# Kernel tuning notes

Hardware: AMD Instinct MI355X
Metric: run time of the kernel (lower is better)

Reference implementation:

```python
import jax, jax.numpy as jnp
import numpy as np

N_NODES = 100000
N_EDGES = 1600000
N_GRAPHS = 256
D = 128
L = 3
N_OUT = 10


def setup_inputs() -> dict:
    key = jax.random.key(0)
    ks = jax.random.split(key, 6)
    x = jax.random.normal(ks[0], (N_NODES, D), dtype=jnp.float32)
    edge_index = jax.random.randint(ks[1], (2, N_EDGES), 0, N_NODES, dtype=jnp.int64)
    batch = jnp.sort(jax.random.randint(ks[2], (N_NODES,), 0, N_GRAPHS, dtype=jnp.int64))
    conv_w = jax.random.normal(ks[3], (L, D, D), dtype=jnp.float32) * (1.0 / np.sqrt(D))
    conv_b = jnp.zeros((L, D), dtype=jnp.float32)
    out_w = jax.random.normal(ks[4], (3 * D, N_OUT), dtype=jnp.float32) * (1.0 / np.sqrt(3 * D))
    out_b = jnp.zeros((N_OUT,), dtype=jnp.float32)
    return {"x": x, "edge_index": edge_index, "batch": batch,
            "conv_w": conv_w, "conv_b": conv_b, "out_w": out_w, "out_b": out_b}


def reference(x, edge_index, batch, conv_w, conv_b, out_w, out_b):
    N = x.shape[0]
    # --- add self-loops (PyG GCNConv default) ---
    loop = jnp.arange(N, dtype=edge_index.dtype)
    src = jnp.concatenate([edge_index[0], loop])  # [E+N]
    dst = jnp.concatenate([edge_index[1], loop])
    # --- symmetric normalization: deg computed on dst (col) ---
    deg = jax.ops.segment_sum(jnp.ones_like(dst, dtype=x.dtype), dst, num_segments=N)
    dinv = jnp.where(deg > 0, jax.lax.rsqrt(jnp.maximum(deg, 1.0)), 0.0)
    norm = dinv[src] * dinv[dst]  # [E+N]

    h = x
    for l in range(conv_w.shape[0]):
        h = h @ conv_w[l]                                   # [N, D] transform first
        msg = h[src] * norm[:, None]                        # gather + scale
        h = jax.ops.segment_sum(msg, dst, num_segments=N)   # scatter-add
        h = jax.nn.relu(h + conv_b[l])

    # --- global max / mean / add pooling over graphs ---
    B = N_GRAPHS
    gmax = jax.ops.segment_max(h, batch, num_segments=B)
    gsum = jax.ops.segment_sum(h, batch, num_segments=B)
    cnt = jax.ops.segment_sum(jnp.ones((N, 1), h.dtype), batch, num_segments=B)
    gmean = gsum / jnp.maximum(cnt, 1.0)
    pooled = jnp.concatenate([gmax, gmean, gsum], axis=1)   # [B, 3D]
    # dropout p=0.5 is identity in eval mode
    return pooled @ out_w + out_b
```

## Files before the change

kernel.cpp:

```cpp
#include <hip/hip_runtime.h>
#include <hip/hip_bf16.h>

#define D 128
#define NP 8
#define DPB 64
#define KPB (DPB * NP)
#define SUB 64
#define CAP_SUB 64

typedef __attribute__((ext_vector_type(8))) __bf16 bf16x8;
typedef __attribute__((ext_vector_type(4))) float f32x4;
typedef __attribute__((ext_vector_type(4))) short s16x4;
typedef __attribute__((ext_vector_type(8))) short s16x8;

static __device__ __forceinline__ short f2bf(float f) {
    union { float f; unsigned u; } in; in.f = f;
    unsigned u = in.u;
    u += 0x7fffu + ((u >> 16) & 1u);
    return (short)(u >> 16);
}

__global__ void k_bucket(const int* __restrict__ src, const int* __restrict__ dst,
                         int* __restrict__ bcnt, int* __restrict__ staging,
                         int E, int KBE,
                         const float* __restrict__ W, short* __restrict__ Wt, int totw,
                         const int* __restrict__ batch, int* __restrict__ gstart,
                         int* __restrict__ gcnt, int N, int B) {
    const int EB = (E + 255) >> 8;
    if (blockIdx.x < (unsigned)EB) {
        int i = blockIdx.x * 256 + threadIdx.x;
        if (i >= E) return;
        int d = __builtin_nontemporal_load(dst + i);
        int s = __builtin_nontemporal_load(src + i);
        int b = d >> 6;
        int key = ((d & 63) << 3) | (s >> 14);
        int j = blockIdx.x & (SUB - 1);
        int slot = atomicAdd(&bcnt[j * KBE + b], 1);
        if (slot < CAP_SUB) staging[((size_t)j * KBE + b) * CAP_SUB + slot] = (key << 17) | s;
    } else if ((int)blockIdx.x - EB < (totw >> 8)) {
        int i = (blockIdx.x - EB) * 256 + threadIdx.x;
        if (i < totw) {
            int l = i >> 14;
            int rem = i & 16383;
            int n = rem >> 7;
            int k = rem & 127;
            Wt[i] = f2bf(W[(l << 14) + (k << 7) + n]);
        }
    } else {
        for (int g = threadIdx.x; g <= B; g += 256) {
            int lo = 0, hi = N;
            while (lo < hi) {
                int mid = (lo + hi) >> 1;
                if (batch[mid] < g) lo = mid + 1; else hi = mid;
            }
            gstart[g] = lo;
            if (g < B) {
                int lo2 = lo, hi2 = N;
                while (lo2 < hi2) {
                    int mid = (lo2 + hi2) >> 1;
                    if (batch[mid] < g + 1) lo2 = mid + 1; else hi2 = mid;
                }
                gcnt[g] = lo2 - lo;
            }
        }
    }
}

__global__ void k_bscan(const int* __restrict__ bcnt, int* __restrict__ bbase,
                        int* __restrict__ row_ptr, int nkeys, int KBE) {
    __shared__ int wtot[8];
    __shared__ int carry_s;
    const int t = threadIdx.x;
    const int w = t >> 6;
    const int lane = t & 63;
    if (t == 0) carry_s = 0;
    __syncthreads();
    for (int c0 = 0; c0 < KBE; c0 += 512) {
        const int b = c0 + t;
        int v = 0;
        if (b < KBE) {
            #pragma unroll 8
            for (int j = 0; j < SUB; j++) {
                int c = bcnt[j * KBE + b];
                v += (c > CAP_SUB) ? CAP_SUB : c;
            }
        }
        int is = v;
        #pragma unroll
        for (int off = 1; off < 64; off <<= 1) {
            int x = __shfl_up(is, off, 64);
            if (lane >= off) is += x;
        }
        if (lane == 63) wtot[w] = is;
        __syncthreads();
        if (t == 0) {
            int run = 0;
            #pragma unroll
            for (int i = 0; i < 8; i++) { int x = wtot[i]; wtot[i] = run; run += x; }
        }
        __syncthreads();
        const int excl = is - v + wtot[w] + carry_s;
        if (b < KBE) bbase[b] = excl;
        __syncthreads();
        if (t == 511) carry_s = excl + v;
        __syncthreads();
    }
    if (t == 0) { bbase[KBE] = carry_s; row_ptr[nkeys] = carry_s; }
}

__global__ __launch_bounds__(256) void k_build(
    const int* __restrict__ staging, const int* __restrict__ bcnt,
    const int* __restrict__ bbase, int* __restrict__ row_ptr,
    int* __restrict__ csr_src, float* __restrict__ dinv, int N, int KBE)
{
    const int b = blockIdx.x;
    const int tid = threadIdx.x;
    __shared__ int cnt[KPB];
    __shared__ int subn[SUB];
    __shared__ int wtot[4];

    if (tid < SUB) {
        int c = bcnt[tid * KBE + b];
        subn[tid] = (c > CAP_SUB) ? CAP_SUB : c;
    }
    for (int k = tid; k < KPB; k += 256) cnt[k] = 0;
    __syncthreads();

    const int base = bbase[b];
    const int nb = bbase[b + 1] - base;
    const int j = tid >> 2, l4 = tid & 3;
    const int* __restrict__ sreg = staging + ((size_t)j * KBE + b) * CAP_SUB;
    const int sn = subn[j];

    for (int e = l4; e < sn; e += 4)
        atomicAdd(&cnt[sreg[e] >> 17], 1);
    __syncthreads();

    {
        const int w = tid >> 6, lane = tid & 63;
        const int e0 = cnt[2 * tid], e1 = cnt[2 * tid + 1];
        const int s = e0 + e1;
        int is = s;
        #pragma unroll
        for (int off = 1; off < 64; off <<= 1) {
            int x = __shfl_up(is, off, 64);
            if (lane >= off) is += x;
        }
        if (lane == 63) wtot[w] = is;
        __syncthreads();
        if (tid == 0) {
            int run = 0;
            #pragma unroll
            for (int i = 0; i < 4; i++) { int x = wtot[i]; wtot[i] = run; run += x; }
        }
        __syncthreads();
        const int excl = is - s + wtot[w];
        cnt[2 * tid] = excl;
        cnt[2 * tid + 1] = excl + e0;
        __syncthreads();
    }

    for (int k = tid; k < KPB; k += 256)
        row_ptr[(size_t)b * KPB + k] = base + cnt[k];
    for (int dl = tid; dl < DPB; dl += 256) {
        int d = b * DPB + dl;
        if (d < N) {
            int hi2 = (dl == DPB - 1) ? nb : cnt[(dl + 1) * NP];
            int deg = hi2 - cnt[dl * NP];
            dinv[d] = rsqrtf((float)deg + 1.0f);
        }
    }
    __syncthreads();

    for (int e = l4; e < sn; e += 4) {
        int w = sreg[e];
        int slot = base + atomicAdd(&cnt[w >> 17], 1);
        csr_src[slot] = w & 0x1FFFF;
    }
}

__global__ void k_cvt_x(const float* __restrict__ x, const float* __restrict__ dinv,
                        short* __restrict__ xb, int total4) {
    int i = blockIdx.x * blockDim.x + threadIdx.x;
    if (i < total4) {
        float d = dinv[i >> 5];
        f32x4 v = __builtin_nontemporal_load((const f32x4*)x + i);
        s16x4 o;
        o.x = f2bf(v.x * d); o.y = f2bf(v.y * d);
        o.z = f2bf(v.z * d); o.w = f2bf(v.w * d);
        ((s16x4*)xb)[i] = o;
    }
}

__global__ __launch_bounds__(256) void k_layer(
    const short* __restrict__ hin, const int* __restrict__ row_ptr,
    const int* __restrict__ csr_src, const float* __restrict__ dinv,
    const short* __restrict__ Wt, const float* __restrict__ bias,
    short* __restrict__ hout, float* __restrict__ hrelu, int N, int mode)
{
    __shared__ __align__(16) short tile[16 * 128];
    const int tid = threadIdx.x;
    const int wave = tid >> 6;
    const int lane = tid & 63;
    const int group = lane >> 4;
    const int lg = lane & 15;
    const int off = lg * 8;
    const int node_base = blockIdx.x * 16;
    const int r = wave * 4 + group;
    const int i = node_base + r;

    short* dstp = &tile[r * 128 + ((lg ^ (r & 7)) << 3)];
    if (i < N) {
        float acc[8];
        bf16x8 v = *(const bf16x8*)(hin + (size_t)i * D + off);
        #pragma unroll
        for (int k = 0; k < 8; k++) acc[k] = (float)v[k];

        int t = row_ptr[i * NP];
        const int end = row_ptr[i * NP + NP];
        const int nfull = (end - t) >> 3;

        int i0, i1, i2, i3, i4, i5, i6, i7;
        if (nfull > 0) {
            i0 = csr_src[t + 0]; i1 = csr_src[t + 1];
            i2 = csr_src[t + 2]; i3 = csr_src[t + 3];
            i4 = csr_src[t + 4]; i5 = csr_src[t + 5];
            i6 = csr_src[t + 6]; i7 = csr_src[t + 7];
        }
        #pragma unroll 1
        for (int c = 0; c < nfull; c++) {
            bf16x8 v0 = *(const bf16x8*)(hin + (size_t)i0 * D + off);
            bf16x8 v1 = *(const bf16x8*)(hin + (size_t)i1 * D + off);
            bf16x8 v2 = *(const bf16x8*)(hin + (size_t)i2 * D + off);
            bf16x8 v3 = *(const bf16x8*)(hin + (size_t)i3 * D + off);
            bf16x8 v4 = *(const bf16x8*)(hin + (size_t)i4 * D + off);
            bf16x8 v5 = *(const bf16x8*)(hin + (size_t)i5 * D + off);
            bf16x8 v6 = *(const bf16x8*)(hin + (size_t)i6 * D + off);
            bf16x8 v7 = *(const bf16x8*)(hin + (size_t)i7 * D + off);
            t += 8;
            if (c + 1 < nfull) {
                i0 = csr_src[t + 0]; i1 = csr_src[t + 1];
                i2 = csr_src[t + 2]; i3 = csr_src[t + 3];
                i4 = csr_src[t + 4]; i5 = csr_src[t + 5];
                i6 = csr_src[t + 6]; i7 = csr_src[t + 7];
            }
            #pragma unroll
            for (int k = 0; k < 8; k++)
                acc[k] += ((((float)v0[k] + (float)v1[k]) + ((float)v2[k] + (float)v3[k]))
                         + (((float)v4[k] + (float)v5[k]) + ((float)v6[k] + (float)v7[k])));
        }
        for (; t + 4 <= end; t += 4) {
            int j0 = csr_src[t + 0], j1 = csr_src[t + 1];
            int j2 = csr_src[t + 2], j3 = csr_src[t + 3];
            bf16x8 v0 = *(const bf16x8*)(hin + (size_t)j0 * D + off);
            bf16x8 v1 = *(const bf16x8*)(hin + (size_t)j1 * D + off);
            bf16x8 v2 = *(const bf16x8*)(hin + (size_t)j2 * D + off);
            bf16x8 v3 = *(const bf16x8*)(hin + (size_t)j3 * D + off);
            #pragma unroll
            for (int k = 0; k < 8; k++)
                acc[k] += (((float)v0[k] + (float)v1[k]) + ((float)v2[k] + (float)v3[k]));
        }
        for (; t < end; t++) {
            int j0 = csr_src[t];
            bf16x8 v0 = *(const bf16x8*)(hin + (size_t)j0 * D + off);
            #pragma unroll
            for (int k = 0; k < 8; k++) acc[k] += (float)v0[k];
        }

        const float di = dinv[i];
        s16x8 o;
        #pragma unroll
        for (int k = 0; k < 8; k++) o[k] = f2bf(acc[k] * di);
        *(s16x8*)dstp = o;
    } else {
        s16x8 z = {0, 0, 0, 0, 0, 0, 0, 0};
        *(s16x8*)dstp = z;
    }
    __syncthreads();

    bf16x8 afrag[4];
    #pragma unroll
    for (int kt = 0; kt < 4; kt++)
        afrag[kt] = *(const bf16x8*)(&tile[lg * 128 + (((group + 4 * kt) ^ (lg & 7)) << 3)]);

    f32x4 acc2[2];
    #pragma unroll
    for (int nt = 0; nt < 2; nt++) { f32x4 z = {0.f, 0.f, 0.f, 0.f}; acc2[nt] = z; }
    #pragma unroll
    for (int nt = 0; nt < 2; nt++) {
        const short* bp = Wt + (size_t)(wave * 32 + nt * 16 + lg) * D + group * 8;
        #pragma unroll
        for (int kt = 0; kt < 4; kt++) {
            bf16x8 b = *(const bf16x8*)(bp + kt * 32);
            acc2[nt] = __builtin_amdgcn_mfma_f32_16x16x32_bf16(afrag[kt], b, acc2[nt], 0, 0, 0);
        }
    }

    float bcol[2];
    #pragma unroll
    for (int nt = 0; nt < 2; nt++) bcol[nt] = bias[wave * 32 + nt * 16 + lg];
    const int row0 = node_base + group * 4;
    #pragma unroll
    for (int i2 = 0; i2 < 4; i2++) {
        int r2 = row0 + i2;
        if (r2 < N) {
            if (mode == 0) {
                float dr = dinv[r2];
                #pragma unroll
                for (int nt = 0; nt < 2; nt++) {
                    int col = wave * 32 + nt * 16 + lg;
                    float val = fmaxf(acc2[nt][i2] + bcol[nt], 0.0f);
                    hout[(size_t)r2 * D + col] = f2bf(val * dr);
                }
            } else {
                #pragma unroll
                for (int nt = 0; nt < 2; nt++) {
                    int col = wave * 32 + nt * 16 + lg;
                    hrelu[(size_t)r2 * D + col] = fmaxf(acc2[nt][i2] + bcol[nt], 0.0f);
                }
            }
        }
    }
}

__global__ __launch_bounds__(256) void k_pool(const float* __restrict__ hrelu,
                                              const int* __restrict__ gstart,
                                              const int* __restrict__ gcnt,
                                              float* __restrict__ pmax,
                                              float* __restrict__ psum, int B) {
    int g = blockIdx.x >> 2;
    int q = blockIdx.x & 3;
    int c = threadIdx.x & 127;
    int p = threadIdx.x >> 7;
    int start = gstart[g];
    int endr = start + gcnt[g];

    float mx0 = 0.f, mx1 = 0.f, sm0 = 0.f, sm1 = 0.f;
    int r = start + q * 2 + p;
    for (; r + 8 < endr; r += 16) {
        float v0 = __builtin_nontemporal_load(hrelu + (size_t)r * D + c);
        float v1 = __builtin_nontemporal_load(hrelu + (size_t)(r + 8) * D + c);
        mx0 = fmaxf(mx0, v0); sm0 += v0;
        mx1 = fmaxf(mx1, v1); sm1 += v1;
    }
    if (r < endr) {
        float v0 = __builtin_nontemporal_load(hrelu + (size_t)r * D + c);
        mx0 = fmaxf(mx0, v0); sm0 += v0;
    }
    float mx = fmaxf(mx0, mx1), sm = sm0 + sm1;

    __shared__ float smx[128], ssm[128];
    if (p == 1) { smx[c] = mx; ssm[c] = sm; }
    __syncthreads();
    if (p == 0) {
        pmax[((size_t)q * B + g) * D + c] = fmaxf(mx, smx[c]);
        psum[((size_t)q * B + g) * D + c] = sm + ssm[c];
    }
}

__global__ void k_final(const float* __restrict__ pmax, const float* __restrict__ psum,
                        const int* __restrict__ gcnt, const float* __restrict__ ow,
                        const float* __restrict__ ob, float* __restrict__ out, int B) {
    int g = blockIdx.x;
    int t = threadIdx.x;
    float part[10];
    #pragma unroll
    for (int o = 0; o < 10; o++) part[o] = 0.f;
    float invc = 1.0f / fmaxf((float)gcnt[g], 1.0f);
    for (int k = t; k < 3 * D; k += 64) {
        int c = (k < D) ? k : ((k < 2 * D) ? k - D : k - 2 * D);
        float pk;
        if (k < D) {
            float m = pmax[(size_t)g * D + c];
            #pragma unroll
            for (int q = 1; q < 4; q++) m = fmaxf(m, pmax[((size_t)q * B + g) * D + c]);
            pk = m;
        } else {
            float s = psum[(size_t)g * D + c];
            #pragma unroll
            for (int q = 1; q < 4; q++) s += psum[((size_t)q * B + g) * D + c];
            pk = (k < 2 * D) ? s * invc : s;
        }
        const float* w = ow + k * 10;
        #pragma unroll
        for (int o = 0; o < 10; o++) part[o] += pk * w[o];
    }
    #pragma unroll
    for (int off = 32; off > 0; off >>= 1)
        #pragma unroll
        for (int o = 0; o < 10; o++) part[o] += __shfl_down(part[o], off, 64);
    if (t == 0)
        #pragma unroll
        for (int o = 0; o < 10; o++) out[g * 10 + o] = part[o] + ob[o];
}

extern "C" void kernel_launch(void* const* d_in, const int* in_sizes, int n_in,
                              void* d_out, int out_size, void* d_ws, size_t ws_size,
                              hipStream_t stream) {
    const float* x     = (const float*)d_in[0];
    const int*   ei    = (const int*)d_in[1];
    const int*   batch = (const int*)d_in[2];
    const float* convw = (const float*)d_in[3];
    const float* convb = (const float*)d_in[4];
    const float* outw  = (const float*)d_in[5];
    const float* outb  = (const float*)d_in[6];
    float* out = (float*)d_out;

    const int N = in_sizes[0] / D;
    const int E = in_sizes[1] / 2;
    const int L = in_sizes[3] / (D * D);
    const int B = out_size / 10;

    const int* src = ei;
    const int* dst = ei + E;

    const int KBE   = (N + DPB - 1) / DPB;
    const int nkeys = KBE * KPB;
    const int totw  = L * D * D;
    const int EB    = (E + 255) / 256;

    char* p = (char*)d_ws;
    auto alloc = [&](size_t bytes) { char* r = p; p += (bytes + 255) & ~255ull; return r; };
    short* hb0     = (short*)alloc((size_t)N * D * 2);
    short* hb1     = (short*)alloc((size_t)N * D * 2);
    float* hrelu   = (float*)alloc((size_t)N * D * 4);
    short* Wt      = (short*)alloc((size_t)L * D * D * 2);
    int*   row_ptr = (int*)alloc(((size_t)nkeys + 1) * 4);
    int*   csr_src = (int*)alloc((size_t)E * 4);
    int*   bcnt    = (int*)alloc((size_t)SUB * KBE * 4);
    int*   bbase   = (int*)alloc(((size_t)KBE + 1) * 4);
    float* dinv    = (float*)alloc((size_t)N * 4);
    float* pmax    = (float*)alloc((size_t)4 * B * D * 4);
    float* psum    = (float*)alloc((size_t)4 * B * D * 4);
    int*   gcnt    = (int*)alloc((size_t)B * 4);
    int*   gstart  = (int*)alloc(((size_t)B + 1) * 4);

    int* staging = (int*)hrelu;

    hipMemsetAsync(bcnt, 0, (size_t)SUB * KBE * 4, stream);

    k_bucket<<<EB + totw / 256 + 1, 256, 0, stream>>>(src, dst, bcnt, staging, E, KBE,
                                                      convw, Wt, totw,
                                                      batch, gstart, gcnt, N, B);
    k_bscan<<<1, 512, 0, stream>>>(bcnt, bbase, row_ptr, nkeys, KBE);
    k_build<<<KBE, 256, 0, stream>>>(staging, bcnt, bbase, row_ptr, csr_src, dinv, N, KBE);
    k_cvt_x<<<((N * D / 4) + 255) / 256, 256, 0, stream>>>(x, dinv, hb0, N * D / 4);

    const int lblocks = (N + 15) / 16;
    k_layer<<<lblocks, 256, 0, stream>>>(hb0, row_ptr, csr_src, dinv, Wt,
                                         convb, hb1, hrelu, N, 0);
    k_layer<<<lblocks, 256, 0, stream>>>(hb1, row_ptr, csr_src, dinv, Wt + D * D,
                                         convb + D, hb0, hrelu, N, 0);
    k_layer<<<lblocks, 256, 0, stream>>>(hb0, row_ptr, csr_src, dinv, Wt + 2 * D * D,
                                         convb + 2 * D, hb1, hrelu, N, 1);

    k_pool<<<B * 4, 256, 0, stream>>>(hrelu, gstart, gcnt, pmax, psum, B);
    k_final<<<B, 64, 0, stream>>>(pmax, psum, gcnt, outw, outb, out, B);
}
```

Before: 454.0 us.

## Replace global bucket scan with atomic cursor and fuse x conversion into build

Removes the single-block k_bscan kernel by having each build block claim its CSR base offset with an atomicAdd on a global cursor. Row pointers become per-bucket segments of KPB+1 entries, so each bucket carries its own end and the layer kernel indexes them by bucket. The separate x-to-bf16 conversion kernel is folded into k_build, which reuses the dinv values it just computed from shared memory. This drops two launches and a serial scan at the cost of nondeterministic CSR segment placement across buckets.

```diff
diff --git a/kernel.cpp b/kernel.cpp
--- a/kernel.cpp
+++ b/kernel.cpp
@@ -5,6 +5,7 @@
 #define NP 8
 #define DPB 64
 #define KPB (DPB * NP)
+#define RPS (KPB + 1)
 #define SUB 64
 #define CAP_SUB 64
 
@@ -66,58 +67,19 @@
     }
 }
 
-__global__ void k_bscan(const int* __restrict__ bcnt, int* __restrict__ bbase,
-                        int* __restrict__ row_ptr, int nkeys, int KBE) {
-    __shared__ int wtot[8];
-    __shared__ int carry_s;
-    const int t = threadIdx.x;
-    const int w = t >> 6;
-    const int lane = t & 63;
-    if (t == 0) carry_s = 0;
-    __syncthreads();
-    for (int c0 = 0; c0 < KBE; c0 += 512) {
-        const int b = c0 + t;
-        int v = 0;
-        if (b < KBE) {
-            #pragma unroll 8
-            for (int j = 0; j < SUB; j++) {
-                int c = bcnt[j * KBE + b];
-                v += (c > CAP_SUB) ? CAP_SUB : c;
-            }
-        }
-        int is = v;
-        #pragma unroll
-        for (int off = 1; off < 64; off <<= 1) {
-            int x = __shfl_up(is, off, 64);
-            if (lane >= off) is += x;
-        }
-        if (lane == 63) wtot[w] = is;
-        __syncthreads();
-        if (t == 0) {
-            int run = 0;
-            #pragma unroll
-            for (int i = 0; i < 8; i++) { int x = wtot[i]; wtot[i] = run; run += x; }
-        }
-        __syncthreads();
-        const int excl = is - v + wtot[w] + carry_s;
-        if (b < KBE) bbase[b] = excl;
-        __syncthreads();
-        if (t == 511) carry_s = excl + v;
-        __syncthreads();
-    }
-    if (t == 0) { bbase[KBE] = carry_s; row_ptr[nkeys] = carry_s; }
-}
-
 __global__ __launch_bounds__(256) void k_build(
     const int* __restrict__ staging, const int* __restrict__ bcnt,
-    const int* __restrict__ bbase, int* __restrict__ row_ptr,
-    int* __restrict__ csr_src, float* __restrict__ dinv, int N, int KBE)
+    int* __restrict__ row_ptr, int* __restrict__ csr_src,
+    float* __restrict__ dinv, int* __restrict__ cursor,
+    const float* __restrict__ x, short* __restrict__ xb, int N, int KBE)
 {
     const int b = blockIdx.x;
     const int tid = threadIdx.x;
     __shared__ int cnt[KPB];
     __shared__ int subn[SUB];
     __shared__ int wtot[4];
+    __shared__ int base_s, tot_s;
+    __shared__ float dinv_s[DPB];
 
     if (tid < SUB) {
         int c = bcnt[tid * KBE + b];
@@ -126,8 +88,6 @@
     for (int k = tid; k < KPB; k += 256) cnt[k] = 0;
     __syncthreads();
 
-    const int base = bbase[b];
-    const int nb = bbase[b + 1] - base;
     const int j = tid >> 2, l4 = tid & 3;
     const int* __restrict__ sreg = staging + ((size_t)j * KBE + b) * CAP_SUB;
     const int sn = subn[j];
@@ -143,52 +103,60 @@
         int is = s;
         #pragma unroll
         for (int off = 1; off < 64; off <<= 1) {
-            int x = __shfl_up(is, off, 64);
-            if (lane >= off) is += x;
+            int xs = __shfl_up(is, off, 64);
+            if (lane >= off) is += xs;
         }
         if (lane == 63) wtot[w] = is;
         __syncthreads();
         if (tid == 0) {
             int run = 0;
             #pragma unroll
-            for (int i = 0; i < 4; i++) { int x = wtot[i]; wtot[i] = run; run += x; }
+            for (int i = 0; i < 4; i++) { int xv = wtot[i]; wtot[i] = run; run += xv; }
         }
         __syncthreads();
         const int excl = is - s + wtot[w];
         cnt[2 * tid] = excl;
         cnt[2 * tid + 1] = excl + e0;
+        if (tid == 255) tot_s = is + wtot[3];
         __syncthreads();
-    }
-
-    for (int k = tid; k < KPB; k += 256)
-        row_ptr[(size_t)b * KPB + k] = base + cnt[k];
+        if (tid == 0) base_s = atomicAdd(cursor, tot_s);
+        __syncthreads();
+    }
+    const int base = base_s;
+    const int tot = tot_s;
+
+    int* __restrict__ rp = row_ptr + (size_t)b * RPS;
+    for (int k = tid; k < KPB; k += 256) rp[k] = base + cnt[k];
+    if (tid == 0) rp[KPB] = base + tot;
     for (int dl = tid; dl < DPB; dl += 256) {
         int d = b * DPB + dl;
         if (d < N) {
-            int hi2 = (dl == DPB - 1) ? nb : cnt[(dl + 1) * NP];
+            int hi2 = (dl == DPB - 1) ? tot : cnt[(dl + 1) * NP];
             int deg = hi2 - cnt[dl * NP];
-            dinv[d] = rsqrtf((float)deg + 1.0f);
+            float dv = rsqrtf((float)deg + 1.0f);
+            dinv[d] = dv;
+            dinv_s[dl] = dv;
         }
     }
     __syncthreads();
 
     for (int e = l4; e < sn; e += 4) {
-        int w = sreg[e];
-        int slot = base + atomicAdd(&cnt[w >> 17], 1);
-        csr_src[slot] = w & 0x1FFFF;
-    }
-}
-
-__global__ void k_cvt_x(const float* __restrict__ x, const float* __restrict__ dinv,
-                        short* __restrict__ xb, int total4) {
-    int i = blockIdx.x * blockDim.x + threadIdx.x;
-    if (i < total4) {
-        float d = dinv[i >> 5];
-        f32x4 v = __builtin_nontemporal_load((const f32x4*)x + i);
-        s16x4 o;
-        o.x = f2bf(v.x * d); o.y = f2bf(v.y * d);
-        o.z = f2bf(v.z * d); o.w = f2bf(v.w * d);
-        ((s16x4*)xb)[i] = o;
+        int wd = sreg[e];
+        int slot = base + atomicAdd(&cnt[wd >> 17], 1);
+        csr_src[slot] = wd & 0x1FFFF;
+    }
+
+    for (int idx = tid; idx < DPB * 32; idx += 256) {
+        const int dl = idx >> 5;
+        const int d = b * DPB + dl;
+        if (d < N) {
+            f32x4 v = __builtin_nontemporal_load((const f32x4*)x + (size_t)d * 32 + (idx & 31));
+            const float dv = dinv_s[dl];
+            s16x4 o;
+            o.x = f2bf(v.x * dv); o.y = f2bf(v.y * dv);
+            o.z = f2bf(v.z * dv); o.w = f2bf(v.w * dv);
+            ((s16x4*)xb)[(size_t)d * 32 + (idx & 31)] = o;
+        }
     }
 }
 
@@ -216,8 +184,9 @@
         #pragma unroll
         for (int k = 0; k < 8; k++) acc[k] = (float)v[k];
 
-        int t = row_ptr[i * NP];
-        const int end = row_ptr[i * NP + NP];
+        const int rb = (i >> 6) * RPS + (i & 63) * NP;
+        int t = row_ptr[rb];
+        const int end = row_ptr[rb + NP];
         const int nfull = (end - t) >> 3;
 
         int i0, i1, i2, i3, i4, i5, i6, i7;
@@ -415,7 +384,6 @@
     const int* dst = ei + E;
 
     const int KBE   = (N + DPB - 1) / DPB;
-    const int nkeys = KBE * KPB;
     const int totw  = L * D * D;
     const int EB    = (E + 255) / 256;
 
@@ -425,26 +393,26 @@
     short* hb1     = (short*)alloc((size_t)N * D * 2);
     float* hrelu   = (float*)alloc((size_t)N * D * 4);
     short* Wt      = (short*)alloc((size_t)L * D * D * 2);
-    int*   row_ptr = (int*)alloc(((size_t)nkeys + 1) * 4);
+    int*   row_ptr = (int*)alloc((size_t)KBE * RPS * 4);
     int*   csr_src = (int*)alloc((size_t)E * 4);
-    int*   bcnt    = (int*)alloc((size_t)SUB * KBE * 4);
-    int*   bbase   = (int*)alloc(((size_t)KBE + 1) * 4);
+    int*   bcnt    = (int*)alloc(((size_t)SUB * KBE + 64) * 4);
     float* dinv    = (float*)alloc((size_t)N * 4);
     float* pmax    = (float*)alloc((size_t)4 * B * D * 4);
     float* psum    = (float*)alloc((size_t)4 * B * D * 4);
     int*   gcnt    = (int*)alloc((size_t)B * 4);
     int*   gstart  = (int*)alloc(((size_t)B + 1) * 4);
 
+    int* cursor = bcnt + (size_t)SUB * KBE;
+
     int* staging = (int*)hrelu;
 
-    hipMemsetAsync(bcnt, 0, (size_t)SUB * KBE * 4, stream);
+    hipMemsetAsync(bcnt, 0, ((size_t)SUB * KBE + 64) * 4, stream);
 
     k_bucket<<<EB + totw / 256 + 1, 256, 0, stream>>>(src, dst, bcnt, staging, E, KBE,
                                                       convw, Wt, totw,
                                                       batch, gstart, gcnt, N, B);
-    k_bscan<<<1, 512, 0, stream>>>(bcnt, bbase, row_ptr, nkeys, KBE);
-    k_build<<<KBE, 256, 0, stream>>>(staging, bcnt, bbase, row_ptr, csr_src, dinv, N, KBE);
-    k_cvt_x<<<((N * D / 4) + 255) / 256, 256, 0, stream>>>(x, dinv, hb0, N * D / 4);
+    k_build<<<KBE, 256, 0, stream>>>(staging, bcnt, row_ptr, csr_src, dinv, cursor,
+                                     x, hb0, N, KBE);
 
     const int lblocks = (N + 15) / 16;
     k_layer<<<lblocks, 256, 0, stream>>>(hb0, row_ptr, csr_src, dinv, Wt,
```

New measurement: 453.8 us. Within noise of the previous version (-0.0%).
